# Performance work log

Measured on AMD Instinct MI355X. Metric: run time of the kernel, lower is better.

The kernel has to match this reference:

```python
import jax, jax.numpy as jnp
import numpy as np

D_MODEL = 1024
NUM_HEADS = 16
HEAD_DIM = D_MODEL // NUM_HEADS


def setup_inputs() -> dict:
    key = jax.random.key(0)
    ks = jax.random.split(key, 11)
    B, S, D = 2, 2048, D_MODEL
    s = 1.0 / np.sqrt(D)
    return {
        "query": jax.random.normal(ks[0], (B, S, D), jnp.float32),
        "key": jax.random.normal(ks[1], (B, S, D), jnp.float32),
        "value": jax.random.normal(ks[2], (B, S, D), jnp.float32),
        "W_q": jax.random.normal(ks[3], (D, D), jnp.float32) * s,
        "b_q": jnp.zeros((D,), jnp.float32),
        "W_k": jax.random.normal(ks[4], (D, D), jnp.float32) * s,
        "b_k": jnp.zeros((D,), jnp.float32),
        "W_v": jax.random.normal(ks[5], (D, D), jnp.float32) * s,
        "b_v": jnp.zeros((D,), jnp.float32),
        "W_o": jax.random.normal(ks[6], (D, D), jnp.float32) * s,
        "b_o": jnp.zeros((D,), jnp.float32),
    }


def reference(query, key, value, W_q, b_q, W_k, b_k, W_v, b_v, W_o, b_o):
    B, S, D = query.shape
    H, Dh = NUM_HEADS, HEAD_DIM
    # linear projections then split heads: [B, S, D] -> [B, H, S, Dh]
    def split_heads(x):
        return x.reshape(B, -1, H, Dh).transpose(0, 2, 1, 3)
    Q = split_heads(query @ W_q.T + b_q)
    K = split_heads(key @ W_k.T + b_k)
    V = split_heads(value @ W_v.T + b_v)
    # NOTE: original scales by d_model**-0.5, not head_dim**-0.5
    scale = jnp.asarray(D, Q.dtype) ** -0.5
    scores = jnp.einsum("bhqd,bhkd->bhqk", Q, K) * scale
    attn = jax.nn.softmax(scores, axis=-1)  # includes max-subtraction stabilization
    out = jnp.einsum("bhqk,bhkd->bhqd", attn, V)
    out = out.transpose(0, 2, 1, 3).reshape(B, -1, D)
    return out @ W_o.T + b_o
```

## Files before the change

kernel.cpp:

```cpp
#include <hip/hip_runtime.h>
#include <stdint.h>


typedef unsigned short u16;
typedef short s16x8 __attribute__((ext_vector_type(8)));
typedef short s16x4 __attribute__((ext_vector_type(4)));
typedef float f32x4 __attribute__((ext_vector_type(4)));
typedef u16 u16x4 __attribute__((ext_vector_type(4)));

#define S_LEN 2048
#define DMODEL 1024
#define LOG2E 1.44269504088896340736f

__device__ __forceinline__ u16 f2bf(float f) {
  union { float f; uint32_t u; } v; v.f = f;
  return (u16)((v.u + 0x8000u) >> 16);
}

__device__ __forceinline__ s16x8 ld8f(const float* s) {
  f32x4 a = *(const f32x4*)s;
  f32x4 b = *(const f32x4*)(s + 4);
  s16x8 r;
  r[0] = (short)f2bf(a[0]); r[1] = (short)f2bf(a[1]);
  r[2] = (short)f2bf(a[2]); r[3] = (short)f2bf(a[3]);
  r[4] = (short)f2bf(b[0]); r[5] = (short)f2bf(b[1]);
  r[6] = (short)f2bf(b[2]); r[7] = (short)f2bf(b[3]);
  return r;
}

__device__ __forceinline__ void gl2lds16(const u16* g, u16* l) {
  __builtin_amdgcn_global_load_lds(
      (const __attribute__((address_space(1))) uint32_t*)g,
      (__attribute__((address_space(3))) uint32_t*)l, 16, 0, 0);
}

struct Cvt7 { const float* s[7]; u16* d[7]; int n[7]; };

__global__ __launch_bounds__(256) void cvt7(Cvt7 p) {
  const int z = blockIdx.y;
  const int idx = blockIdx.x * 256 + threadIdx.x;
  if (idx * 8 < p.n[z])
    *(s16x8*)(p.d[z] + (size_t)idx * 8) = ld8f(p.s[z] + (size_t)idx * 8);
}

struct GemmBatch {
  const u16* A[3]; const u16* W[3]; const float* Bv[3]; void* C[3];
  u16* vt;
  float scl[3];
};

template <int BM, int BN, bool OUT_F32, bool VT>
__global__ __launch_bounds__(256) void gemm_bt(GemmBatch p, int M, int N, int K) {
  static_assert(!VT || (BM == 128 && BN == 128), "VT epilogue assumes 128x128");
  constexpr int MI = BM / 32, NJ = BN / 32;
  constexpr int TS = BM + 8;
  constexpr int AB = BM * 64 + BN * 64;
  constexpr int TB = VT ? BN * TS : 0;
  constexpr int SM = AB > TB ? AB : TB;
  __shared__ u16 smem[SM];
  u16* const As = smem;
  u16* const Ws = smem + BM * 64;

  const int z = blockIdx.z;
  const u16* __restrict__ A      = p.A[z];
  const u16* __restrict__ W      = p.W[z];
  const float* __restrict__ bias = p.Bv[z];
  const float scl = p.scl[z];

  const int tid = threadIdx.x;
  const int wave = tid >> 6, lane = tid & 63;
  const int quad = lane >> 4, l16 = lane & 15;
  const int bm = blockIdx.y * BM, bn = blockIdx.x * BN;
  const int wr = (wave >> 1) * (BM / 2), wc = (wave & 1) * (BN / 2);
  const int sr8 = lane >> 3;
  const int slc = (lane & 7) ^ sr8;
  const int srow = wave * 8 + sr8;

  f32x4 acc[MI][NJ];
#pragma unroll
  for (int i = 0; i < MI; i++)
#pragma unroll
    for (int j = 0; j < NJ; j++) acc[i][j] = {0.f, 0.f, 0.f, 0.f};

  const u16* Ab = A + (size_t)bm * K;
  const u16* Wb = W + (size_t)bn * K;

  for (int kt = 0; kt < K; kt += 64) {
    __syncthreads();
#pragma unroll
    for (int i = 0; i < MI; i++)
      gl2lds16(Ab + (size_t)(i * 32 + srow) * K + kt + slc * 8,
               &As[(i * 32 + wave * 8) * 64]);
#pragma unroll
    for (int i = 0; i < NJ; i++)
      gl2lds16(Wb + (size_t)(i * 32 + srow) * K + kt + slc * 8,
               &Ws[(i * 32 + wave * 8) * 64]);
    __syncthreads();

#pragma unroll
    for (int ks = 0; ks < 2; ks++) {
      const int ch = ks * 4 + quad;
      s16x8 a[MI], b[NJ];
#pragma unroll
      for (int t = 0; t < MI; t++)
        a[t] = *(const s16x8*)&As[(wr + t * 16 + l16) * 64 + ((ch ^ (l16 & 7)) << 3)];
#pragma unroll
      for (int t = 0; t < NJ; t++)
        b[t] = *(const s16x8*)&Ws[(wc + t * 16 + l16) * 64 + ((ch ^ (l16 & 7)) << 3)];
#pragma unroll
      for (int i = 0; i < MI; i++)
#pragma unroll
        for (int j = 0; j < NJ; j++)
          acc[i][j] = __builtin_amdgcn_mfma_f32_16x16x32_bf16(a[i], b[j], acc[i][j], 0, 0, 0);
    }
  }

  if (VT && z == 2) {
    __syncthreads();
    u16* const T = smem;
#pragma unroll
    for (int j = 0; j < NJ; j++) {
      const int c = wc + j * 16 + l16;
      const float bv = bias[bn + c];
#pragma unroll
      for (int i = 0; i < MI; i++) {
        const int r0 = wr + i * 16 + quad * 4;
        u16x4 t4;
#pragma unroll
        for (int r = 0; r < 4; r++) t4[r] = f2bf((acc[i][j][r] + bv) * scl);
        *(u16x4*)&T[c * TS + r0] = t4;
      }
    }
    __syncthreads();
    const int c = tid >> 1, half = tid & 1;
    const int b_ = bm >> 11;
    const int sb = (bm & 2047) + half * 64;
    u16* dst = p.vt + (size_t)(b_ * 1024 + bn + c) * S_LEN + sb;
    const u16* srcT = &T[c * TS + half * 64];
#pragma unroll
    for (int k = 0; k < 8; k++)
      *(s16x8*)(dst + k * 8) = *(const s16x8*)(srcT + k * 8);
  } else {
#pragma unroll
    for (int j = 0; j < NJ; j++) {
      const int col = bn + wc + j * 16 + l16;
      const float bv = bias[col];
#pragma unroll
      for (int i = 0; i < MI; i++) {
        const int row0 = bm + wr + i * 16 + quad * 4;
#pragma unroll
        for (int r = 0; r < 4; r++) {
          const float val = (acc[i][j][r] + bv) * scl;
          if (OUT_F32)
            ((float*)p.C[z])[(size_t)(row0 + r) * N + col] = val;
          else
            ((u16*)p.C[z])[(size_t)(row0 + r) * N + col] = f2bf(val);
        }
      }
    }
  }
}

__global__ __launch_bounds__(512, 4) void attn_kernel(const u16* __restrict__ Qp,
                                                      const u16* __restrict__ Kp,
                                                      const u16* __restrict__ Vt,
                                                      u16* __restrict__ AO) {
  __shared__ u16 smem[24576];
  u16* const Qs = smem;
  u16* const Ks = smem + 8192;
  u16* const Vs = smem + 16384;

  const int tid = threadIdx.x;
  const int wave = tid >> 6, lane = tid & 63;
  const int quad = lane >> 4, l16 = lane & 15;
  const int bh = blockIdx.y, b = bh >> 4, h = bh & 15;
  const int s0 = blockIdx.x * 128;
  const int qw = wave & 3;
  const int kvh = wave >> 2;

  const int sr = tid >> 3, sc8 = tid & 7;
  const int sxor = (sc8 ^ (sr & 7)) << 3;
  const int vr = tid >> 4, vc = tid & 15;
  const int vxor = (vc ^ (vr & 15)) << 3;

#pragma unroll
  for (int i = 0; i < 2; i++) {
    const int rr = i * 64 + sr;
    s16x8 qv = *(const s16x8*)(Qp + (size_t)(b * S_LEN + s0 + rr) * DMODEL + h * 64 + sc8 * 8);
    *(s16x8*)&Qs[rr * 64 + sxor] = qv;
  }
  __syncthreads();

  s16x8 aq[2][2];
#pragma unroll
  for (int ks = 0; ks < 2; ks++)
#pragma unroll
    for (int rt = 0; rt < 2; rt++) {
      const int row = qw * 32 + rt * 16 + l16;
      const int ch = ks * 4 + quad;
      aq[ks][rt] = *(const s16x8*)&Qs[row * 64 + ((ch ^ (l16 & 7)) << 3)];
    }

  s16x8 kv[2], vv[2];
#pragma unroll
  for (int i = 0; i < 2; i++)
    kv[i] = *(const s16x8*)(Kp + (size_t)(b * S_LEN + i * 64 + sr) * DMODEL + h * 64 + sc8 * 8);
#pragma unroll
  for (int i = 0; i < 2; i++)
    vv[i] = *(const s16x8*)(Vt + (size_t)(bh * 64 + i * 32 + vr) * S_LEN + vc * 8);

  f32x4 o[2][4];
  float l_r[2] = {0.f, 0.f};
#pragma unroll
  for (int rt = 0; rt < 2; rt++)
#pragma unroll
    for (int dt = 0; dt < 4; dt++) o[rt][dt] = {0.f, 0.f, 0.f, 0.f};

  const f32x4 zf = {0.f, 0.f, 0.f, 0.f};

  for (int kt = 0; kt < S_LEN; kt += 128) {
    __syncthreads();
#pragma unroll
    for (int i = 0; i < 2; i++)
      *(s16x8*)&Ks[(i * 64 + sr) * 64 + sxor] = kv[i];
#pragma unroll
    for (int i = 0; i < 2; i++)
      *(s16x8*)&Vs[(i * 32 + vr) * 128 + vxor] = vv[i];
    __syncthreads();

    if (kt + 128 < S_LEN) {
      const int k2 = kt + 128;
#pragma unroll
      for (int i = 0; i < 2; i++)
        kv[i] = *(const s16x8*)(Kp + (size_t)(b * S_LEN + k2 + i * 64 + sr) * DMODEL + h * 64 + sc8 * 8);
#pragma unroll
      for (int i = 0; i < 2; i++)
        vv[i] = *(const s16x8*)(Vt + (size_t)(bh * 64 + i * 32 + vr) * S_LEN + k2 + vc * 8);
    }

#pragma unroll
    for (int kvt = 0; kvt < 4; kvt++) {
      const int krow = kvh * 64 + kvt * 16 + l16;
      s16x8 ak0 = *(const s16x8*)&Ks[krow * 64 + (((0 + quad) ^ (l16 & 7)) << 3)];
      s16x8 ak1 = *(const s16x8*)&Ks[krow * 64 + (((4 + quad) ^ (l16 & 7)) << 3)];

      s16x4 pf[2];
#pragma unroll
      for (int rt = 0; rt < 2; rt++) {
        f32x4 sA;
        sA = __builtin_amdgcn_mfma_f32_16x16x32_bf16(ak0, aq[0][rt], zf, 0, 0, 0);
        sA = __builtin_amdgcn_mfma_f32_16x16x32_bf16(ak1, aq[1][rt], sA, 0, 0, 0);

        union { float f; uint32_t u; } e0, e1, e2, e3;
        e0.f = __builtin_amdgcn_exp2f(sA[0]);
        e1.f = __builtin_amdgcn_exp2f(sA[1]);
        e2.f = __builtin_amdgcn_exp2f(sA[2]);
        e3.f = __builtin_amdgcn_exp2f(sA[3]);
        l_r[rt] += (((e0.f + e1.f) + e2.f) + e3.f);

        union { uint32_t u[2]; s16x4 v; } pk;
        pk.u[0] = __builtin_amdgcn_perm(e1.u + 0x8000u, e0.u + 0x8000u, 0x07060302u);
        pk.u[1] = __builtin_amdgcn_perm(e3.u + 0x8000u, e2.u + 0x8000u, 0x07060302u);
        pf[rt] = pk.v;
      }

      const int ch = kvh * 8 + kvt * 2 + (quad >> 1);
#pragma unroll
      for (int dt = 0; dt < 4; dt++) {
        const int row = dt * 16 + l16;
        s16x4 bv = *(const s16x4*)&Vs[row * 128 + ((ch ^ l16) << 3) + (quad & 1) * 4];
        o[0][dt] = __builtin_amdgcn_mfma_f32_16x16x16bf16_1k(pf[0], bv, o[0][dt], 0, 0, 0);
        o[1][dt] = __builtin_amdgcn_mfma_f32_16x16x16bf16_1k(pf[1], bv, o[1][dt], 0, 0, 0);
      }
    }
  }

#pragma unroll
  for (int rt = 0; rt < 2; rt++) {
    l_r[rt] += __shfl_xor(l_r[rt], 16);
    l_r[rt] += __shfl_xor(l_r[rt], 32);
  }

  __syncthreads();
  f32x4* const mrgO = (f32x4*)smem;
  float* const mrgL = (float*)smem + 8192;
  if (wave >= 4) {
    const int w = wave - 4;
#pragma unroll
    for (int rt = 0; rt < 2; rt++) {
#pragma unroll
      for (int dt = 0; dt < 4; dt++)
        mrgO[(rt * 4 + dt) * 256 + w * 64 + lane] = o[rt][dt];
      mrgL[rt * 256 + w * 64 + lane] = l_r[rt];
    }
  }
  __syncthreads();
  if (wave < 4) {
#pragma unroll
    for (int rt = 0; rt < 2; rt++) {
#pragma unroll
      for (int dt = 0; dt < 4; dt++) {
        f32x4 ov = mrgO[(rt * 4 + dt) * 256 + wave * 64 + lane];
        o[rt][dt] += ov;
      }
      l_r[rt] += mrgL[rt * 256 + wave * 64 + lane];
    }
#pragma unroll
    for (int rt = 0; rt < 2; rt++) {
#pragma unroll
      for (int r = 0; r < 4; r++) {
        const float linv = 1.f / __shfl(l_r[rt], quad * 4 + r);
        const int row = s0 + qw * 32 + rt * 16 + quad * 4 + r;
#pragma unroll
        for (int dt = 0; dt < 4; dt++)
          AO[(size_t)(b * S_LEN + row) * DMODEL + h * 64 + dt * 16 + l16] =
              f2bf(o[rt][dt][r] * linv);
      }
    }
  }
}

extern "C" void kernel_launch(void* const* d_in, const int* in_sizes, int n_in,
                              void* d_out, int out_size, void* d_ws, size_t ws_size,
                              hipStream_t stream) {
  const float* query = (const float*)d_in[0];
  const float* key_  = (const float*)d_in[1];
  const float* value = (const float*)d_in[2];
  const float* W_q = (const float*)d_in[3];
  const float* b_q = (const float*)d_in[4];
  const float* W_k = (const float*)d_in[5];
  const float* b_k = (const float*)d_in[6];
  const float* W_v = (const float*)d_in[7];
  const float* b_v = (const float*)d_in[8];
  const float* W_o = (const float*)d_in[9];
  const float* b_o = (const float*)d_in[10];
  float* out = (float*)d_out;

  const int M = 2 * S_LEN;
  const int N = DMODEL, K = DMODEL;
  const size_t WSZ = (size_t)DMODEL * DMODEL;
  const size_t SZ  = (size_t)M * DMODEL;

  u16* Wqb = (u16*)d_ws;
  u16* Wkb = Wqb + WSZ;
  u16* Wvb = Wkb + WSZ;
  u16* Wob = Wvb + WSZ;
  u16* Qa  = Wob + WSZ;
  u16* Ka  = Qa + SZ;
  u16* Va  = Ka + SZ;
  u16* Qp  = Va + SZ;
  u16* Kp  = Qp + SZ;
  u16* Vt  = Kp + SZ;
  u16* AO  = Qp;

  Cvt7 cw;
  cw.s[0] = W_q;   cw.d[0] = Wqb; cw.n[0] = (int)WSZ;
  cw.s[1] = W_k;   cw.d[1] = Wkb; cw.n[1] = (int)WSZ;
  cw.s[2] = W_v;   cw.d[2] = Wvb; cw.n[2] = (int)WSZ;
  cw.s[3] = W_o;   cw.d[3] = Wob; cw.n[3] = (int)WSZ;
  cw.s[4] = query; cw.d[4] = Qa;  cw.n[4] = (int)SZ;
  cw.s[5] = key_;  cw.d[5] = Ka;  cw.n[5] = (int)SZ;
  cw.s[6] = value; cw.d[6] = Va;  cw.n[6] = (int)SZ;
  cvt7<<<dim3((int)(SZ / 2048), 7), 256, 0, stream>>>(cw);

  GemmBatch p1;
  p1.A[0] = Qa; p1.W[0] = Wqb; p1.Bv[0] = b_q; p1.C[0] = Qp;
  p1.A[1] = Ka; p1.W[1] = Wkb; p1.Bv[1] = b_k; p1.C[1] = Kp;
  p1.A[2] = Va; p1.W[2] = Wvb; p1.Bv[2] = b_v; p1.C[2] = Vt;
  p1.vt = Vt;
  p1.scl[0] = 0.03125f * LOG2E;
  p1.scl[1] = 1.0f;
  p1.scl[2] = 1.0f;
  gemm_bt<128, 128, false, true><<<dim3(N / 128, M / 128, 3), 256, 0, stream>>>(p1, M, N, K);

  attn_kernel<<<dim3(S_LEN / 128, 32), 512, 0, stream>>>(Qp, Kp, Vt, AO);

  GemmBatch p2;
  p2.A[0] = AO; p2.W[0] = Wob; p2.Bv[0] = b_o; p2.C[0] = out;
  p2.A[1] = AO; p2.W[1] = Wob; p2.Bv[1] = b_o; p2.C[1] = out;
  p2.A[2] = AO; p2.W[2] = Wob; p2.Bv[2] = b_o; p2.C[2] = out;
  p2.vt = nullptr;
  p2.scl[0] = 1.0f; p2.scl[1] = 1.0f; p2.scl[2] = 1.0f;
  gemm_bt<64, 64, true, false><<<dim3(N / 64, M / 64, 1), 256, 0, stream>>>(p2, M, N, K);
}
```

Baseline: 227.8 us.

## Shrink attention query tile to 64 rows and split KV across four wave groups

The attention block now covers 64 query rows instead of 128. Its 8 waves are arranged as 2 query groups by 4 KV-split groups, and partial outputs are merged with a two-stage tree reduction through shared memory. This doubles the grid to 1024 blocks and lowers shared memory per block, which should improve occupancy and load balance across CUs. The cost is that each K/V tile is reused by half as many query rows, so K/V global and LDS traffic per unit of work doubles, and the epilogue gains extra reduction and barrier steps.

```diff
diff --git a/kernel.cpp b/kernel.cpp
--- a/kernel.cpp
+++ b/kernel.cpp
@@ -161,33 +161,31 @@
   }
 }
 
-__global__ __launch_bounds__(512, 4) void attn_kernel(const u16* __restrict__ Qp,
+__global__ __launch_bounds__(512, 8) void attn_kernel(const u16* __restrict__ Qp,
                                                       const u16* __restrict__ Kp,
                                                       const u16* __restrict__ Vt,
                                                       u16* __restrict__ AO) {
-  __shared__ u16 smem[24576];
+  __shared__ u16 smem[20480];
   u16* const Qs = smem;
-  u16* const Ks = smem + 8192;
-  u16* const Vs = smem + 16384;
+  u16* const Ks = smem + 4096;
+  u16* const Vs = smem + 12288;
 
   const int tid = threadIdx.x;
   const int wave = tid >> 6, lane = tid & 63;
   const int quad = lane >> 4, l16 = lane & 15;
   const int bh = blockIdx.y, b = bh >> 4, h = bh & 15;
-  const int s0 = blockIdx.x * 128;
-  const int qw = wave & 3;
-  const int kvh = wave >> 2;
+  const int s0 = blockIdx.x * 64;
+  const int qw = wave & 1;
+  const int kvq = wave >> 1;
 
   const int sr = tid >> 3, sc8 = tid & 7;
   const int sxor = (sc8 ^ (sr & 7)) << 3;
   const int vr = tid >> 4, vc = tid & 15;
   const int vxor = (vc ^ (vr & 15)) << 3;
 
-#pragma unroll
-  for (int i = 0; i < 2; i++) {
-    const int rr = i * 64 + sr;
-    s16x8 qv = *(const s16x8*)(Qp + (size_t)(b * S_LEN + s0 + rr) * DMODEL + h * 64 + sc8 * 8);
-    *(s16x8*)&Qs[rr * 64 + sxor] = qv;
+  {
+    s16x8 qv = *(const s16x8*)(Qp + (size_t)(b * S_LEN + s0 + sr) * DMODEL + h * 64 + sc8 * 8);
+    *(s16x8*)&Qs[sr * 64 + sxor] = qv;
   }
   __syncthreads();
 
@@ -239,8 +237,8 @@
     }
 
 #pragma unroll
-    for (int kvt = 0; kvt < 4; kvt++) {
-      const int krow = kvh * 64 + kvt * 16 + l16;
+    for (int kvt = 0; kvt < 2; kvt++) {
+      const int krow = kvq * 32 + kvt * 16 + l16;
       s16x8 ak0 = *(const s16x8*)&Ks[krow * 64 + (((0 + quad) ^ (l16 & 7)) << 3)];
       s16x8 ak1 = *(const s16x8*)&Ks[krow * 64 + (((4 + quad) ^ (l16 & 7)) << 3)];
 
@@ -264,7 +262,7 @@
         pf[rt] = pk.v;
       }
 
-      const int ch = kvh * 8 + kvt * 2 + (quad >> 1);
+      const int ch = kvq * 4 + kvt * 2 + (quad >> 1);
 #pragma unroll
       for (int dt = 0; dt < 4; dt++) {
         const int row = dt * 16 + l16;
@@ -281,36 +279,57 @@
     l_r[rt] += __shfl_xor(l_r[rt], 32);
   }
 
+  f32x4* const mrgO = (f32x4*)smem;
+  float* const mrgL = (float*)(smem + 16384);
   __syncthreads();
-  f32x4* const mrgO = (f32x4*)smem;
-  float* const mrgL = (float*)smem + 8192;
   if (wave >= 4) {
-    const int w = wave - 4;
+    const int slot = wave - 4;
 #pragma unroll
     for (int rt = 0; rt < 2; rt++) {
 #pragma unroll
       for (int dt = 0; dt < 4; dt++)
-        mrgO[(rt * 4 + dt) * 256 + w * 64 + lane] = o[rt][dt];
-      mrgL[rt * 256 + w * 64 + lane] = l_r[rt];
+        mrgO[(slot * 8 + rt * 4 + dt) * 64 + lane] = o[rt][dt];
+      mrgL[(slot * 2 + rt) * 64 + lane] = l_r[rt];
     }
   }
   __syncthreads();
   if (wave < 4) {
-#pragma unroll
-    for (int rt = 0; rt < 2; rt++) {
-#pragma unroll
-      for (int dt = 0; dt < 4; dt++) {
-        f32x4 ov = mrgO[(rt * 4 + dt) * 256 + wave * 64 + lane];
-        o[rt][dt] += ov;
-      }
-      l_r[rt] += mrgL[rt * 256 + wave * 64 + lane];
+    const int slot = wave;
+#pragma unroll
+    for (int rt = 0; rt < 2; rt++) {
+#pragma unroll
+      for (int dt = 0; dt < 4; dt++)
+        o[rt][dt] += mrgO[(slot * 8 + rt * 4 + dt) * 64 + lane];
+      l_r[rt] += mrgL[(slot * 2 + rt) * 64 + lane];
+    }
+  }
+  __syncthreads();
+  if (wave >= 2 && wave < 4) {
+    const int slot = wave - 2;
+#pragma unroll
+    for (int rt = 0; rt < 2; rt++) {
+#pragma unroll
+      for (int dt = 0; dt < 4; dt++)
+        mrgO[(slot * 8 + rt * 4 + dt) * 64 + lane] = o[rt][dt];
+      mrgL[(slot * 2 + rt) * 64 + lane] = l_r[rt];
+    }
+  }
+  __syncthreads();
+  if (wave < 2) {
+    const int slot = wave;
+#pragma unroll
+    for (int rt = 0; rt < 2; rt++) {
+#pragma unroll
+      for (int dt = 0; dt < 4; dt++)
+        o[rt][dt] += mrgO[(slot * 8 + rt * 4 + dt) * 64 + lane];
+      l_r[rt] += mrgL[(slot * 2 + rt) * 64 + lane];
     }
 #pragma unroll
     for (int rt = 0; rt < 2; rt++) {
 #pragma unroll
       for (int r = 0; r < 4; r++) {
         const float linv = 1.f / __shfl(l_r[rt], quad * 4 + r);
-        const int row = s0 + qw * 32 + rt * 16 + quad * 4 + r;
+        const int row = s0 + wave * 32 + rt * 16 + quad * 4 + r;
 #pragma unroll
         for (int dt = 0; dt < 4; dt++)
           AO[(size_t)(b * S_LEN + row) * DMODEL + h * 64 + dt * 16 + l16] =
@@ -373,7 +392,7 @@
   p1.scl[2] = 1.0f;
   gemm_bt<128, 128, false, true><<<dim3(N / 128, M / 128, 3), 256, 0, stream>>>(p1, M, N, K);
 
-  attn_kernel<<<dim3(S_LEN / 128, 32), 512, 0, stream>>>(Qp, Kp, Vt, AO);
+  attn_kernel<<<dim3(S_LEN / 64, 32), 512, 0, stream>>>(Qp, Kp, Vt, AO);
 
   GemmBatch p2;
   p2.A[0] = AO; p2.W[0] = Wob; p2.Bv[0] = b_o; p2.C[0] = out;
```

New measurement: 814.8 us. 258% more time.
